# Optimization experiments

Measured on AMD Instinct MI355X. Metric: run time of the kernel, lower is better.

## Reference

```python
import jax, jax.numpy as jnp
import numpy as np

E, B, F, L = 4, 8192, 2048, 100  # envs, batch/env, feature dim, num classes
LAM = 1.0  # hparams['RERM_lam']


def setup_inputs() -> dict:
    key = jax.random.key(0)
    k1, k2, k3 = jax.random.split(key, 3)
    feats = jax.random.normal(k1, (E, B, F), jnp.float32)
    y = jax.random.randint(k2, (E, B), 0, L)
    W = jax.random.normal(k3, (F, L), jnp.float32) * 0.02
    b = jnp.zeros((L,), jnp.float32)
    return {"feats": feats, "y": y, "W": W, "b": b}


def _rerm_loss(feats, y, W, b):
    # --- per-(label, env) masked means (mean_table / visit_table) ---
    onehot = jax.nn.one_hot(y, L, dtype=feats.dtype)          # [E,B,L]
    counts = onehot.sum(axis=1)                               # [E,L]
    sums = jnp.einsum('ebl,ebf->elf', onehot, feats)          # [E,L,F]
    means = sums / jnp.maximum(counts, 1.0)[..., None]        # [E,L,F]
    visit = (counts > 0).astype(feats.dtype)                  # [E,L]

    # --- torch.var(mean_table[i, fetch_envs, :], dim=1): variance over
    # feature dim per env (unbiased, /(F-1)), then mean over visited envs ---
    mu = means.mean(axis=-1, keepdims=True)                   # [E,L,1]
    var = jnp.sum((means - mu) ** 2, axis=-1) / (F - 1)       # [E,L]

    nvis = visit.sum(axis=0)                                  # [L]
    sel = (nvis > 1.5).astype(feats.dtype)                    # labels with >1 env
    per_label = (var * visit).sum(axis=0) / jnp.maximum(nvis, 1.0)  # [L]
    nzlabel = jnp.maximum(sel.sum(), 1.0)
    mean_loss = LAM * jnp.sum(per_label * sel) / nzlabel

    # --- cross-entropy over all envs concatenated ---
    logits = feats.reshape(E * B, F) @ W + b                  # [E*B,L]
    logp = jax.nn.log_softmax(logits, axis=-1)
    ce = -jnp.take_along_axis(logp, y.reshape(-1, 1), axis=1).mean()

    return mean_loss + ce


def reference(feats, y, W, b):
    return _rerm_loss(feats, y, W, b)
```

## Files before the change

### kernel.cpp

```cpp
#include <hip/hip_runtime.h>
#include <hip/hip_bf16.h>
#include <math.h>

#define E 4
#define B 8192
#define F 2048
#define L 100
#define NROWS (E * B)
#define LAMBDA 1.0f

typedef __attribute__((ext_vector_type(8))) short bf16x8;
typedef __attribute__((ext_vector_type(4))) float f32x4;

static __device__ inline unsigned short f2bf(float x) {
    unsigned u = __float_as_uint(x);
    unsigned r = (u + 0x7FFFu + ((u >> 16) & 1u)) >> 16;
    return (unsigned short)r;
}

#define SG 4
#define NSG 25
#define SBS 8
#define SRW (B / SBS)
#define NSUM (E * SBS * NSG)

#define GBM 128
#define GNC 112
#define GKC 64
#define APAD 72
#define NGEMM (NROWS / GBM)
#define NUNIT (NGEMM + NSUM)
#define KMB 512

__global__ void __launch_bounds__(256) k_prep(const float* __restrict__ W,
                                              unsigned short* __restrict__ Wt,
                                              float* __restrict__ ce_accum,
                                              int* __restrict__ counts,
                                              int* __restrict__ ctr) {
    __shared__ float st[64][101];
    int t = threadIdx.x;
    int b = blockIdx.x;
    if (b == 0) {
        for (int i = t; i < E * L; i += 256) counts[i] = 0;
        if (t == 0) { ce_accum[0] = 0.f; ctr[0] = 0; }
    }
    int k0 = b * 64;
    for (int i = t; i < 64 * 100; i += 256) {
        st[i / 100][i % 100] = W[(size_t)k0 * L + i];
    }
    __syncthreads();
    for (int i = t; i < 112 * 32; i += 256) {
        int n = i >> 5, kp = i & 31;
        unsigned lo = 0, hi = 0;
        if (n < L) {
            lo = f2bf(st[kp * 2][n]);
            hi = f2bf(st[kp * 2 + 1][n]);
        }
        *(unsigned*)&Wt[(size_t)n * F + k0 + kp * 2] = lo | (hi << 16);
    }
}

static __device__ inline unsigned pack_bf(float lo, float hi) {
    unsigned ul = __float_as_uint(lo) + 0x8000u;
    unsigned uh = __float_as_uint(hi) + 0x8000u;
    return __builtin_amdgcn_perm(uh, ul, 0x07060302u);
}

__global__ void __launch_bounds__(512, 4) k_main(const float* __restrict__ feats,
                                                 const int* __restrict__ y,
                                                 const unsigned short* __restrict__ Wt,
                                                 const float* __restrict__ bias,
                                                 float* __restrict__ partial,
                                                 int* __restrict__ counts,
                                                 float* __restrict__ ce_accum,
                                                 int* __restrict__ ctr) {
    __shared__ __align__(16) char sm[34624];
    __shared__ int s_unit;
    int t = threadIdx.x;

    for (;;) {
        __syncthreads();
        if (t == 0) s_unit = atomicAdd(ctr, 1);
        __syncthreads();
        int u = s_unit;
        if (u >= NUNIT) break;

        if (u < NGEMM) {
            unsigned short* As = (unsigned short*)sm;
            unsigned short* Ws = As + GBM * APAD;
            float* red = (float*)(sm + 34560);
            int wave = t >> 6, lane = t & 63;
            int quad = lane >> 4, l16 = lane & 15;
            size_t row0 = (size_t)u * GBM;

            f32x4 acc[7];
#pragma unroll
            for (int ct = 0; ct < 7; ++ct) acc[ct] = (f32x4){0.f, 0.f, 0.f, 0.f};

            int srow = t >> 2;
            int sq = t & 3;

            const float* aptr = feats + (row0 + srow) * (size_t)F + sq * 16;
            const unsigned short* wptr = Wt + (size_t)srow * F + sq * 16;

            float4 pa[4];
            uint4 pw[2];
#pragma unroll
            for (int i = 0; i < 4; ++i) pa[i] = ((const float4*)aptr)[i];
            if (srow < GNC) {
#pragma unroll
                for (int i = 0; i < 2; ++i) pw[i] = ((const uint4*)wptr)[i];
            }

            for (int k0 = 0; k0 < F; k0 += GKC) {
                unsigned uu[8];
#pragma unroll
                for (int i = 0; i < 4; ++i) {
                    uu[i * 2]     = pack_bf(pa[i].x, pa[i].y);
                    uu[i * 2 + 1] = pack_bf(pa[i].z, pa[i].w);
                }
                *(uint4*)&As[srow * APAD + sq * 16]     = make_uint4(uu[0], uu[1], uu[2], uu[3]);
                *(uint4*)&As[srow * APAD + sq * 16 + 8] = make_uint4(uu[4], uu[5], uu[6], uu[7]);
                if (srow < GNC) {
                    *(uint4*)&Ws[srow * APAD + sq * 16] = pw[0];
                    *(uint4*)&Ws[srow * APAD + sq * 16 + 8] = pw[1];
                }
                __syncthreads();

                if (k0 + GKC < F) {
                    const float* ap = aptr + k0 + GKC;
                    const unsigned short* wp = wptr + k0 + GKC;
#pragma unroll
                    for (int i = 0; i < 4; ++i) pa[i] = ((const float4*)ap)[i];
                    if (srow < GNC) {
#pragma unroll
                        for (int i = 0; i < 2; ++i) pw[i] = ((const uint4*)wp)[i];
                    }
                }

#pragma unroll
                for (int ks = 0; ks < 2; ++ks) {
                    bf16x8 bfr = *(const bf16x8*)&As[(wave * 16 + l16) * APAD + ks * 32 + quad * 8];
#pragma unroll
                    for (int ct = 0; ct < 7; ++ct) {
                        bf16x8 af = *(const bf16x8*)&Ws[(ct * 16 + l16) * APAD + ks * 32 + quad * 8];
                        acc[ct] = __builtin_amdgcn_mfma_f32_16x16x32_bf16(af, bfr, acc[ct], 0, 0, 0);
                    }
                }
                __syncthreads();
            }

            int grow = (int)row0 + wave * 16 + l16;
            int lab = y[grow];
            float vv[7][4];
            float vm = -1e30f;
#pragma unroll
            for (int ct = 0; ct < 7; ++ct) {
#pragma unroll
                for (int r = 0; r < 4; ++r) {
                    int c = ct * 16 + quad * 4 + r;
                    float bb = (c < L) ? bias[c] : 0.f;
                    float v = acc[ct][r] + bb;
                    vv[ct][r] = v;
                    if (c < L) vm = fmaxf(vm, v);
                }
            }
            vm = fmaxf(vm, __shfl_xor(vm, 16));
            vm = fmaxf(vm, __shfl_xor(vm, 32));
            float se = 0.f, tv = 0.f;
#pragma unroll
            for (int ct = 0; ct < 7; ++ct) {
#pragma unroll
                for (int r = 0; r < 4; ++r) {
                    int c = ct * 16 + quad * 4 + r;
                    if (c < L) se += __expf(vv[ct][r] - vm);
                    if (c == lab) tv = vv[ct][r];
                }
            }
            se += __shfl_xor(se, 16);
            se += __shfl_xor(se, 32);
            tv += __shfl_xor(tv, 16);
            tv += __shfl_xor(tv, 32);
            float ce = vm + __logf(se) - tv;
#pragma unroll
            for (int s = 1; s <= 8; s <<= 1) ce += __shfl_xor(ce, s);
            if (lane == 0) red[wave] = ce;
            __syncthreads();
            if (t == 0) {
                float v = 0.f;
#pragma unroll
                for (int w = 0; w < 8; ++w) v += red[w];
                atomicAdd(ce_accum, v);
            }
        } else {
            int* ys = (int*)sm;
            unsigned short* list = (unsigned short*)(sm + 4096);
            int* cnt4 = (int*)(sm + 4096 + 2048);
            int* ntot = (int*)(sm + 4096 + 2048 + 16);
            int bi = u - NGEMM;
            int lg = bi % NSG;
            int bs = (bi / NSG) % SBS;
            int e  = bi / (NSG * SBS);
            int lab0 = lg * SG;

            if (t < SG) cnt4[t] = 0;
            if (t == 8) ntot[0] = 0;
            const int* yb = y + e * B + bs * SRW;
            ys[t] = yb[t];
            ys[t + 512] = yb[t + 512];
            __syncthreads();

            for (int r = t; r < SRW; r += 512) {
                int lb = ys[r] - lab0;
                if ((unsigned)lb < SG) {
                    atomicAdd(&cnt4[lb], 1);
                    int p = atomicAdd(ntot, 1);
                    list[p] = (unsigned short)(r | (lb << 10));
                }
            }
            __syncthreads();
            int n = ntot[0];
            int npad = (n + 3) & ~3;
            if (t < npad - n) list[n + t] = 0;
            __syncthreads();

            const float* fb = feats + ((size_t)e * B + (size_t)bs * SRW) * F + t * 4;
            float4 a0 = make_float4(0.f, 0.f, 0.f, 0.f);
            float4 a1 = a0, a2 = a0, a3 = a0;

            float4 x[4];
            int tg[4];
            if (n > 0) {
#pragma unroll
                for (int j = 0; j < 4; ++j) {
                    int ev = list[j];
                    tg[j] = ev >> 10;
                    x[j] = *(const float4*)(fb + (size_t)(ev & 1023) * F);
                }
                for (int i = 0; i < npad; i += 4) {
                    float4 nx[4];
                    int ntg[4];
                    if (i + 4 < npad) {
#pragma unroll
                        for (int j = 0; j < 4; ++j) {
                            int ev = list[i + 4 + j];
                            ntg[j] = ev >> 10;
                            nx[j] = *(const float4*)(fb + (size_t)(ev & 1023) * F);
                        }
                    }
#pragma unroll
                    for (int j = 0; j < 4; ++j) {
                        if (i + j < n) {
                            float4 v = x[j];
                            int g = tg[j];
                            if (g == 0)      { a0.x += v.x; a0.y += v.y; a0.z += v.z; a0.w += v.w; }
                            else if (g == 1) { a1.x += v.x; a1.y += v.y; a1.z += v.z; a1.w += v.w; }
                            else if (g == 2) { a2.x += v.x; a2.y += v.y; a2.z += v.z; a2.w += v.w; }
                            else             { a3.x += v.x; a3.y += v.y; a3.z += v.z; a3.w += v.w; }
                        }
                    }
#pragma unroll
                    for (int j = 0; j < 4; ++j) { x[j] = nx[j]; tg[j] = ntg[j]; }
                }
            }

            float* pb = partial + (((size_t)e * SBS + bs) * L + lab0) * F + t * 4;
            *(float4*)(pb + 0 * F) = a0;
            *(float4*)(pb + 1 * F) = a1;
            *(float4*)(pb + 2 * F) = a2;
            *(float4*)(pb + 3 * F) = a3;
            if (t < SG) atomicAdd(&counts[e * L + lab0 + t], cnt4[t]);
        }
    }
}

__global__ void __launch_bounds__(512) k_var(const float* __restrict__ partial,
                                             const int* __restrict__ counts,
                                             float* __restrict__ var_out) {
    int el = blockIdx.x;
    int e = el / L, l = el % L;
    int t = threadIdx.x;
    float inv = 1.f / fmaxf((float)counts[el], 1.f);
    float4 s = make_float4(0.f, 0.f, 0.f, 0.f);
#pragma unroll
    for (int bs = 0; bs < SBS; ++bs) {
        float4 v = *(const float4*)&partial[(((size_t)e * SBS + bs) * L + l) * F + t * 4];
        s.x += v.x; s.y += v.y; s.z += v.z; s.w += v.w;
    }
    float mx = s.x * inv, my = s.y * inv, mz = s.z * inv, mw = s.w * inv;
    float sm = mx + my + mz + mw;
    float sm2 = mx * mx + my * my + mz * mz + mw * mw;
#pragma unroll
    for (int sft = 1; sft <= 32; sft <<= 1) {
        sm += __shfl_xor(sm, sft);
        sm2 += __shfl_xor(sm2, sft);
    }
    __shared__ float r1[8], r2[8];
    int wv = t >> 6, ln = t & 63;
    if (ln == 0) { r1[wv] = sm; r2[wv] = sm2; }
    __syncthreads();
    if (t == 0) {
        float S = 0.f, S2 = 0.f;
#pragma unroll
        for (int w = 0; w < 8; ++w) { S += r1[w]; S2 += r2[w]; }
        var_out[el] = (S2 - S * S / (float)F) / (float)(F - 1);
    }
}

__global__ void k_final(const int* __restrict__ counts,
                        const float* __restrict__ var_in,
                        const float* __restrict__ ce_accum,
                        float* __restrict__ out) {
    __shared__ float s_sum[128], s_cnt[128];
    int t = threadIdx.x;
    float selsum = 0.f, selcnt = 0.f;
    for (int l = t; l < L; l += 128) {
        float nvis = 0.f, vsum = 0.f;
        for (int e = 0; e < E; ++e) {
            if (counts[e * L + l] > 0) { nvis += 1.f; vsum += var_in[e * L + l]; }
        }
        float per_label = vsum / fmaxf(nvis, 1.f);
        if (nvis > 1.5f) { selsum += per_label; selcnt += 1.f; }
    }
    s_sum[t] = selsum; s_cnt[t] = selcnt;
    __syncthreads();
    for (int s = 64; s > 0; s >>= 1) {
        if (t < s) { s_sum[t] += s_sum[t + s]; s_cnt[t] += s_cnt[t + s]; }
        __syncthreads();
    }
    if (t == 0) {
        float mean_loss = LAMBDA * s_sum[0] / fmaxf(s_cnt[0], 1.f);
        float ce = ce_accum[0] / (float)NROWS;
        out[0] = mean_loss + ce;
    }
}

extern "C" void kernel_launch(void* const* d_in, const int* in_sizes, int n_in,
                              void* d_out, int out_size, void* d_ws, size_t ws_size,
                              hipStream_t stream) {
    const float* feats = (const float*)d_in[0];
    const int*   y     = (const int*)d_in[1];
    const float* Wm    = (const float*)d_in[2];
    const float* bias  = (const float*)d_in[3];
    float* out = (float*)d_out;

    char* ws = (char*)d_ws;
    float*          ce_accum = (float*)ws;
    int*            ctr      = (int*)(ws + 64);
    int*            counts   = (int*)(ws + 256);
    float*          var_buf  = (float*)(ws + 2048);
    float*          partial  = (float*)(ws + 4096);
    unsigned short* Wt       = (unsigned short*)(ws + 4096 + (size_t)E * SBS * L * F * 4);

    k_prep<<<F / 64, 256, 0, stream>>>(Wm, Wt, ce_accum, counts, ctr);
    k_main<<<KMB, 512, 0, stream>>>(feats, y, Wt, bias, partial, counts, ce_accum, ctr);
    k_var<<<E * L, 512, 0, stream>>>(partial, counts, var_buf);
    k_final<<<1, 128, 0, stream>>>(counts, var_buf, ce_accum, out);
}
```

Baseline: 444.9 us.

## Drop LDS staging in GEMM and replace persistent work queue with static grid

```diff
diff --git a/kernel.cpp b/kernel.cpp
--- a/kernel.cpp
+++ b/kernel.cpp
@@ -25,24 +25,18 @@
 #define NSUM (E * SBS * NSG)
 
 #define GBM 128
-#define GNC 112
-#define GKC 64
-#define APAD 72
 #define NGEMM (NROWS / GBM)
-#define NUNIT (NGEMM + NSUM)
-#define KMB 512
 
 __global__ void __launch_bounds__(256) k_prep(const float* __restrict__ W,
                                               unsigned short* __restrict__ Wt,
                                               float* __restrict__ ce_accum,
-                                              int* __restrict__ counts,
-                                              int* __restrict__ ctr) {
+                                              int* __restrict__ counts) {
     __shared__ float st[64][101];
     int t = threadIdx.x;
     int b = blockIdx.x;
     if (b == 0) {
         for (int i = t; i < E * L; i += 256) counts[i] = 0;
-        if (t == 0) { ce_accum[0] = 0.f; ctr[0] = 0; }
+        if (t == 0) ce_accum[0] = 0.f;
     }
     int k0 = b * 64;
     for (int i = t; i < 64 * 100; i += 256) {
@@ -72,205 +66,163 @@
                                                  const float* __restrict__ bias,
                                                  float* __restrict__ partial,
                                                  int* __restrict__ counts,
-                                                 float* __restrict__ ce_accum,
-                                                 int* __restrict__ ctr) {
-    __shared__ __align__(16) char sm[34624];
-    __shared__ int s_unit;
+                                                 float* __restrict__ ce_accum) {
+    __shared__ __align__(16) char sm[6208];
     int t = threadIdx.x;
 
-    for (;;) {
-        __syncthreads();
-        if (t == 0) s_unit = atomicAdd(ctr, 1);
-        __syncthreads();
-        int u = s_unit;
-        if (u >= NUNIT) break;
-
-        if (u < NGEMM) {
-            unsigned short* As = (unsigned short*)sm;
-            unsigned short* Ws = As + GBM * APAD;
-            float* red = (float*)(sm + 34560);
-            int wave = t >> 6, lane = t & 63;
-            int quad = lane >> 4, l16 = lane & 15;
-            size_t row0 = (size_t)u * GBM;
-
-            f32x4 acc[7];
-#pragma unroll
-            for (int ct = 0; ct < 7; ++ct) acc[ct] = (f32x4){0.f, 0.f, 0.f, 0.f};
-
-            int srow = t >> 2;
-            int sq = t & 3;
-
-            const float* aptr = feats + (row0 + srow) * (size_t)F + sq * 16;
-            const unsigned short* wptr = Wt + (size_t)srow * F + sq * 16;
-
-            float4 pa[4];
-            uint4 pw[2];
-#pragma unroll
-            for (int i = 0; i < 4; ++i) pa[i] = ((const float4*)aptr)[i];
-            if (srow < GNC) {
-#pragma unroll
-                for (int i = 0; i < 2; ++i) pw[i] = ((const uint4*)wptr)[i];
-            }
-
-            for (int k0 = 0; k0 < F; k0 += GKC) {
-                unsigned uu[8];
-#pragma unroll
-                for (int i = 0; i < 4; ++i) {
-                    uu[i * 2]     = pack_bf(pa[i].x, pa[i].y);
-                    uu[i * 2 + 1] = pack_bf(pa[i].z, pa[i].w);
-                }
-                *(uint4*)&As[srow * APAD + sq * 16]     = make_uint4(uu[0], uu[1], uu[2], uu[3]);
-                *(uint4*)&As[srow * APAD + sq * 16 + 8] = make_uint4(uu[4], uu[5], uu[6], uu[7]);
-                if (srow < GNC) {
-                    *(uint4*)&Ws[srow * APAD + sq * 16] = pw[0];
-                    *(uint4*)&Ws[srow * APAD + sq * 16 + 8] = pw[1];
-                }
-                __syncthreads();
-
-                if (k0 + GKC < F) {
-                    const float* ap = aptr + k0 + GKC;
-                    const unsigned short* wp = wptr + k0 + GKC;
-#pragma unroll
-                    for (int i = 0; i < 4; ++i) pa[i] = ((const float4*)ap)[i];
-                    if (srow < GNC) {
-#pragma unroll
-                        for (int i = 0; i < 2; ++i) pw[i] = ((const uint4*)wp)[i];
+    if (blockIdx.x < NGEMM) {
+        float* red = (float*)sm;
+        int wave = t >> 6, lane = t & 63;
+        int quad = lane >> 4, l16 = lane & 15;
+        int row = blockIdx.x * GBM + wave * 16 + l16;
+        const float* ap = feats + (size_t)row * F + quad * 8;
+        const unsigned short* wbase = Wt + (size_t)l16 * F + quad * 8;
+
+        f32x4 acc[7];
+#pragma unroll
+        for (int ct = 0; ct < 7; ++ct) acc[ct] = (f32x4){0.f, 0.f, 0.f, 0.f};
+
+        float4 na0 = ((const float4*)ap)[0];
+        float4 na1 = ((const float4*)ap)[1];
+#pragma unroll 2
+        for (int kk = 0; kk < F / 32; ++kk) {
+            float4 a0 = na0, a1 = na1;
+            if (kk + 1 < F / 32) {
+                const float* apn = ap + (size_t)(kk + 1) * 32;
+                na0 = ((const float4*)apn)[0];
+                na1 = ((const float4*)apn)[1];
+            }
+            union { unsigned w[4]; bf16x8 v; } bb;
+            bb.w[0] = pack_bf(a0.x, a0.y);
+            bb.w[1] = pack_bf(a0.z, a0.w);
+            bb.w[2] = pack_bf(a1.x, a1.y);
+            bb.w[3] = pack_bf(a1.z, a1.w);
+#pragma unroll
+            for (int ct = 0; ct < 7; ++ct) {
+                bf16x8 af = *(const bf16x8*)(wbase + (size_t)ct * 16 * F + kk * 32);
+                acc[ct] = __builtin_amdgcn_mfma_f32_16x16x32_bf16(af, bb.v, acc[ct], 0, 0, 0);
+            }
+        }
+
+        int lab = y[row];
+        float vv[7][4];
+        float vm = -1e30f;
+#pragma unroll
+        for (int ct = 0; ct < 7; ++ct) {
+#pragma unroll
+            for (int r = 0; r < 4; ++r) {
+                int c = ct * 16 + quad * 4 + r;
+                float bb2 = (c < L) ? bias[c] : 0.f;
+                float v = acc[ct][r] + bb2;
+                vv[ct][r] = v;
+                if (c < L) vm = fmaxf(vm, v);
+            }
+        }
+        vm = fmaxf(vm, __shfl_xor(vm, 16));
+        vm = fmaxf(vm, __shfl_xor(vm, 32));
+        float se = 0.f, tv = 0.f;
+#pragma unroll
+        for (int ct = 0; ct < 7; ++ct) {
+#pragma unroll
+            for (int r = 0; r < 4; ++r) {
+                int c = ct * 16 + quad * 4 + r;
+                if (c < L) se += __expf(vv[ct][r] - vm);
+                if (c == lab) tv = vv[ct][r];
+            }
+        }
+        se += __shfl_xor(se, 16);
+        se += __shfl_xor(se, 32);
+        tv += __shfl_xor(tv, 16);
+        tv += __shfl_xor(tv, 32);
+        float ce = vm + __logf(se) - tv;
+#pragma unroll
+        for (int s = 1; s <= 8; s <<= 1) ce += __shfl_xor(ce, s);
+        if (lane == 0) red[wave] = ce;
+        __syncthreads();
+        if (t == 0) {
+            float v = 0.f;
+#pragma unroll
+            for (int w = 0; w < 8; ++w) v += red[w];
+            atomicAdd(ce_accum, v);
+        }
+    } else {
+        int* ys = (int*)sm;
+        unsigned short* list = (unsigned short*)(sm + 4096);
+        int* cnt4 = (int*)(sm + 4096 + 2048);
+        int* ntot = (int*)(sm + 4096 + 2048 + 16);
+        int bi = blockIdx.x - NGEMM;
+        int lg = bi % NSG;
+        int bs = (bi / NSG) % SBS;
+        int e  = bi / (NSG * SBS);
+        int lab0 = lg * SG;
+
+        if (t < SG) cnt4[t] = 0;
+        if (t == 8) ntot[0] = 0;
+        const int* yb = y + e * B + bs * SRW;
+        ys[t] = yb[t];
+        ys[t + 512] = yb[t + 512];
+        __syncthreads();
+
+        for (int r = t; r < SRW; r += 512) {
+            int lb = ys[r] - lab0;
+            if ((unsigned)lb < SG) {
+                atomicAdd(&cnt4[lb], 1);
+                int p = atomicAdd(ntot, 1);
+                list[p] = (unsigned short)(r | (lb << 10));
+            }
+        }
+        __syncthreads();
+        int n = ntot[0];
+        int npad = (n + 3) & ~3;
+        if (t < npad - n) list[n + t] = 0;
+        __syncthreads();
+
+        const float* fb = feats + ((size_t)e * B + (size_t)bs * SRW) * F + t * 4;
+        float4 a0 = make_float4(0.f, 0.f, 0.f, 0.f);
+        float4 a1 = a0, a2 = a0, a3 = a0;
+
+        float4 x[4];
+        int tg[4];
+        if (n > 0) {
+#pragma unroll
+            for (int j = 0; j < 4; ++j) {
+                int ev = list[j];
+                tg[j] = ev >> 10;
+                x[j] = *(const float4*)(fb + (size_t)(ev & 1023) * F);
+            }
+            for (int i = 0; i < npad; i += 4) {
+                float4 nx[4];
+                int ntg[4];
+                if (i + 4 < npad) {
+#pragma unroll
+                    for (int j = 0; j < 4; ++j) {
+                        int ev = list[i + 4 + j];
+                        ntg[j] = ev >> 10;
+                        nx[j] = *(const float4*)(fb + (size_t)(ev & 1023) * F);
                     }
                 }
-
-#pragma unroll
-                for (int ks = 0; ks < 2; ++ks) {
-                    bf16x8 bfr = *(const bf16x8*)&As[(wave * 16 + l16) * APAD + ks * 32 + quad * 8];
-#pragma unroll
-                    for (int ct = 0; ct < 7; ++ct) {
-                        bf16x8 af = *(const bf16x8*)&Ws[(ct * 16 + l16) * APAD + ks * 32 + quad * 8];
-                        acc[ct] = __builtin_amdgcn_mfma_f32_16x16x32_bf16(af, bfr, acc[ct], 0, 0, 0);
+#pragma unroll
+                for (int j = 0; j < 4; ++j) {
+                    if (i + j < n) {
+                        float4 v = x[j];
+                        int g = tg[j];
+                        if (g == 0)      { a0.x += v.x; a0.y += v.y; a0.z += v.z; a0.w += v.w; }
+                        else if (g == 1) { a1.x += v.x; a1.y += v.y; a1.z += v.z; a1.w += v.w; }
+                        else if (g == 2) { a2.x += v.x; a2.y += v.y; a2.z += v.z; a2.w += v.w; }
+                        else             { a3.x += v.x; a3.y += v.y; a3.z += v.z; a3.w += v.w; }
                     }
                 }
-                __syncthreads();
-            }
-
-            int grow = (int)row0 + wave * 16 + l16;
-            int lab = y[grow];
-            float vv[7][4];
-            float vm = -1e30f;
-#pragma unroll
-            for (int ct = 0; ct < 7; ++ct) {
-#pragma unroll
-                for (int r = 0; r < 4; ++r) {
-                    int c = ct * 16 + quad * 4 + r;
-                    float bb = (c < L) ? bias[c] : 0.f;
-                    float v = acc[ct][r] + bb;
-                    vv[ct][r] = v;
-                    if (c < L) vm = fmaxf(vm, v);
-                }
-            }
-            vm = fmaxf(vm, __shfl_xor(vm, 16));
-            vm = fmaxf(vm, __shfl_xor(vm, 32));
-            float se = 0.f, tv = 0.f;
-#pragma unroll
-            for (int ct = 0; ct < 7; ++ct) {
-#pragma unroll
-                for (int r = 0; r < 4; ++r) {
-                    int c = ct * 16 + quad * 4 + r;
-                    if (c < L) se += __expf(vv[ct][r] - vm);
-                    if (c == lab) tv = vv[ct][r];
-                }
-            }
-            se += __shfl_xor(se, 16);
-            se += __shfl_xor(se, 32);
-            tv += __shfl_xor(tv, 16);
-            tv += __shfl_xor(tv, 32);
-            float ce = vm + __logf(se) - tv;
-#pragma unroll
-            for (int s = 1; s <= 8; s <<= 1) ce += __shfl_xor(ce, s);
-            if (lane == 0) red[wave] = ce;
-            __syncthreads();
-            if (t == 0) {
-                float v = 0.f;
-#pragma unroll
-                for (int w = 0; w < 8; ++w) v += red[w];
-                atomicAdd(ce_accum, v);
-            }
-        } else {
-            int* ys = (int*)sm;
-            unsigned short* list = (unsigned short*)(sm + 4096);
-            int* cnt4 = (int*)(sm + 4096 + 2048);
-            int* ntot = (int*)(sm + 4096 + 2048 + 16);
-            int bi = u - NGEMM;
-            int lg = bi % NSG;
-            int bs = (bi / NSG) % SBS;
-            int e  = bi / (NSG * SBS);
-            int lab0 = lg * SG;
-
-            if (t < SG) cnt4[t] = 0;
-            if (t == 8) ntot[0] = 0;
-            const int* yb = y + e * B + bs * SRW;
-            ys[t] = yb[t];
-            ys[t + 512] = yb[t + 512];
-            __syncthreads();
-
-            for (int r = t; r < SRW; r += 512) {
-                int lb = ys[r] - lab0;
-                if ((unsigned)lb < SG) {
-                    atomicAdd(&cnt4[lb], 1);
-                    int p = atomicAdd(ntot, 1);
-                    list[p] = (unsigned short)(r | (lb << 10));
-                }
-            }
-            __syncthreads();
-            int n = ntot[0];
-            int npad = (n + 3) & ~3;
-            if (t < npad - n) list[n + t] = 0;
-            __syncthreads();
-
-            const float* fb = feats + ((size_t)e * B + (size_t)bs * SRW) * F + t * 4;
-            float4 a0 = make_float4(0.f, 0.f, 0.f, 0.f);
-            float4 a1 = a0, a2 = a0, a3 = a0;
-
-            float4 x[4];
-            int tg[4];
-            if (n > 0) {
-#pragma unroll
-                for (int j = 0; j < 4; ++j) {
-                    int ev = list[j];
-                    tg[j] = ev >> 10;
-                    x[j] = *(const float4*)(fb + (size_t)(ev & 1023) * F);
-                }
-                for (int i = 0; i < npad; i += 4) {
-                    float4 nx[4];
-                    int ntg[4];
-                    if (i + 4 < npad) {
-#pragma unroll
-                        for (int j = 0; j < 4; ++j) {
-                            int ev = list[i + 4 + j];
-                            ntg[j] = ev >> 10;
-                            nx[j] = *(const float4*)(fb + (size_t)(ev & 1023) * F);
-                        }
-                    }
-#pragma unroll
-                    for (int j = 0; j < 4; ++j) {
-                        if (i + j < n) {
-                            float4 v = x[j];
-                            int g = tg[j];
-                            if (g == 0)      { a0.x += v.x; a0.y += v.y; a0.z += v.z; a0.w += v.w; }
-                            else if (g == 1) { a1.x += v.x; a1.y += v.y; a1.z += v.z; a1.w += v.w; }
-                            else if (g == 2) { a2.x += v.x; a2.y += v.y; a2.z += v.z; a2.w += v.w; }
-                            else             { a3.x += v.x; a3.y += v.y; a3.z += v.z; a3.w += v.w; }
-                        }
-                    }
-#pragma unroll
-                    for (int j = 0; j < 4; ++j) { x[j] = nx[j]; tg[j] = ntg[j]; }
-                }
-            }
-
-            float* pb = partial + (((size_t)e * SBS + bs) * L + lab0) * F + t * 4;
-            *(float4*)(pb + 0 * F) = a0;
-            *(float4*)(pb + 1 * F) = a1;
-            *(float4*)(pb + 2 * F) = a2;
-            *(float4*)(pb + 3 * F) = a3;
-            if (t < SG) atomicAdd(&counts[e * L + lab0 + t], cnt4[t]);
-        }
+#pragma unroll
+                for (int j = 0; j < 4; ++j) { x[j] = nx[j]; tg[j] = ntg[j]; }
+            }
+        }
+
+        float* pb = partial + (((size_t)e * SBS + bs) * L + lab0) * F + t * 4;
+        *(float4*)(pb + 0 * F) = a0;
+        *(float4*)(pb + 1 * F) = a1;
+        *(float4*)(pb + 2 * F) = a2;
+        *(float4*)(pb + 3 * F) = a3;
+        if (t < SG) atomicAdd(&counts[e * L + lab0 + t], cnt4[t]);
     }
 }
 
@@ -346,14 +298,13 @@
 
     char* ws = (char*)d_ws;
     float*          ce_accum = (float*)ws;
-    int*            ctr      = (int*)(ws + 64);
     int*            counts   = (int*)(ws + 256);
     float*          var_buf  = (float*)(ws + 2048);
     float*          partial  = (float*)(ws + 4096);
     unsigned short* Wt       = (unsigned short*)(ws + 4096 + (size_t)E * SBS * L * F * 4);
 
-    k_prep<<<F / 64, 256, 0, stream>>>(Wm, Wt, ce_accum, counts, ctr);
-    k_main<<<KMB, 512, 0, stream>>>(feats, y, Wt, bias, partial, counts, ce_accum, ctr);
+    k_prep<<<F / 64, 256, 0, stream>>>(Wm, Wt, ce_accum, counts);
+    k_main<<<NGEMM + NSUM, 512, 0, stream>>>(feats, y, Wt, bias, partial, counts, ce_accum);
     k_var<<<E * L, 512, 0, stream>>>(partial, counts, var_buf);
     k_final<<<1, 128, 0, stream>>>(counts, var_buf, ce_accum, out);
 }
```

Result: slower. 491.6 us (+10.5%).
